# Performance work log

Measured on AMD Instinct MI355X. Metric: run time of the kernel, lower is better.

## Reference

```python
import jax, jax.numpy as jnp
import numpy as np

N_NODES = 100000
N_EDGES = 600000
IN_SIZE = 128
OUT_SIZE = 128
N_GRAPHS = 100
BN_EPS = 1e-5


def setup_inputs() -> dict:
    key = jax.random.key(0)
    ks = jax.random.split(key, 8)
    h = jax.random.normal(ks[0], (N_NODES, IN_SIZE), dtype=jnp.float32)
    norm = jax.random.uniform(ks[1], (N_NODES, 1), dtype=jnp.float32)
    src = jax.random.randint(ks[2], (N_EDGES,), 0, N_NODES, dtype=jnp.int32)
    dst = jax.random.randint(ks[3], (N_EDGES,), 0, N_NODES, dtype=jnp.int32)
    graph_ids = jnp.sort(jax.random.randint(ks[4], (N_NODES,), 0, N_GRAPHS, dtype=jnp.int32))
    # Linear + BatchNorm params
    W = jax.random.normal(ks[5], (IN_SIZE, OUT_SIZE), dtype=jnp.float32) / np.sqrt(IN_SIZE)
    b = jnp.zeros((OUT_SIZE,), dtype=jnp.float32)
    gamma = jnp.ones((OUT_SIZE,), dtype=jnp.float32)
    beta = jnp.zeros((OUT_SIZE,), dtype=jnp.float32)
    return {"h": h, "norm": norm, "W": W, "b": b, "gamma": gamma, "beta": beta,
            "src": src, "dst": dst, "graph_ids": graph_ids}


def reference(h, norm, W, b, gamma, beta, src, dst, graph_ids):
    # pre-normalize, scatter-sum over edges (copy_src + sum), post-normalize
    x = h * norm                                            # [N, in]
    agg = jax.ops.segment_sum(x[src], dst, num_segments=N_NODES)  # SpMM
    x = agg * norm
    # linear + relu
    x = jax.nn.relu(jnp.dot(x, W) + b)                      # [N, out]
    # BatchNorm1d (training-mode: batch mean, biased variance)
    mean = jnp.mean(x, axis=0)
    var = jnp.mean(jnp.square(x - mean), axis=0)
    x = (x - mean) * jax.lax.rsqrt(var + BN_EPS) * gamma + beta
    # sum_nodes pooling per graph
    phis = jax.ops.segment_sum(x, graph_ids, num_segments=N_GRAPHS)  # [G, out]
    return (x, phis)
```

## Files before the change

### kernel.cpp

```cpp
#include <hip/hip_runtime.h>
#include <hip/hip_bf16.h>

#define N_NODES 100000
#define N_PAD 100096
#define N_EDGES 600000
#define CH 128
#define N_GRAPHS 100
#define BN_EPS 1e-5f
#define NBUCKET 64
#define CAP 32
#define OVFCAP 8192
#define FILL_BLOCKS 586
#define PRESCALE_BLOCKS 6250

typedef __bf16 bf16x8 __attribute__((ext_vector_type(8)));
typedef float f32x4 __attribute__((ext_vector_type(4)));

__device__ __forceinline__ ushort f2bf(float f) {
    union { float f; unsigned u; } x; x.f = f;
    unsigned u = x.u;
    unsigned r = (u + 0x7fffu + ((u >> 16) & 1u)) >> 16;
    return (ushort)r;
}
__device__ __forceinline__ float bflo(unsigned p) { return __builtin_bit_cast(float, p << 16); }
__device__ __forceinline__ float bfhi(unsigned p) { return __builtin_bit_cast(float, p & 0xffff0000u); }

__global__ __launch_bounds__(256) void k_front(const int* __restrict__ src,
        const int* __restrict__ dst, const float* __restrict__ h,
        const float* __restrict__ norm, const float* __restrict__ W,
        int* __restrict__ cnt, int* __restrict__ ovfcur, int* __restrict__ ovf,
        int* __restrict__ esrc, ushort* __restrict__ xh, ushort* __restrict__ Wt) {
    unsigned bid = blockIdx.x;
    if (bid < FILL_BLOCKS) {
        int e0 = (bid * 256 + threadIdx.x) * 4;
        if (e0 < N_EDGES) {
            int4 d = *(const int4*)(dst + e0);
            int4 s = *(const int4*)(src + e0);
            int s0 = atomicAdd(&cnt[d.x], 1);
            int s1 = atomicAdd(&cnt[d.y], 1);
            int s2 = atomicAdd(&cnt[d.z], 1);
            int s3 = atomicAdd(&cnt[d.w], 1);
            if (s0 < CAP) esrc[d.x * CAP + s0] = s.x;
            else { int p = atomicAdd(ovfcur, 1); if (p < OVFCAP) { ovf[2*p] = d.x; ovf[2*p+1] = s.x; } }
            if (s1 < CAP) esrc[d.y * CAP + s1] = s.y;
            else { int p = atomicAdd(ovfcur, 1); if (p < OVFCAP) { ovf[2*p] = d.y; ovf[2*p+1] = s.y; } }
            if (s2 < CAP) esrc[d.z * CAP + s2] = s.z;
            else { int p = atomicAdd(ovfcur, 1); if (p < OVFCAP) { ovf[2*p] = d.z; ovf[2*p+1] = s.z; } }
            if (s3 < CAP) esrc[d.w * CAP + s3] = s.w;
            else { int p = atomicAdd(ovfcur, 1); if (p < OVFCAP) { ovf[2*p] = d.w; ovf[2*p+1] = s.w; } }
        }
    } else if (bid < FILL_BLOCKS + PRESCALE_BLOCKS) {
        int t = (bid - FILL_BLOCKS) * 256 + threadIdx.x;
        int n = t >> 4, c = (t & 15) << 3;
        float nm = norm[n];
        float4 a = *(const float4*)(h + (size_t)n * CH + c);
        float4 d = *(const float4*)(h + (size_t)n * CH + c + 4);
        uint4 o;
        o.x = (unsigned)f2bf(a.x * nm) | ((unsigned)f2bf(a.y * nm) << 16);
        o.y = (unsigned)f2bf(a.z * nm) | ((unsigned)f2bf(a.w * nm) << 16);
        o.z = (unsigned)f2bf(d.x * nm) | ((unsigned)f2bf(d.y * nm) << 16);
        o.w = (unsigned)f2bf(d.z * nm) | ((unsigned)f2bf(d.w * nm) << 16);
        *(uint4*)(xh + (size_t)n * CH + c) = o;
    } else {
        int t = (bid - FILL_BLOCKS - PRESCALE_BLOCKS) * 256 + threadIdx.x;
        int k = t >> 7, o = t & 127;
        Wt[o * CH + k] = f2bf(W[t]);
    }
}

__global__ __launch_bounds__(256) void k_gather(const ushort* __restrict__ xh,
        const float* __restrict__ norm, const int* __restrict__ cnt,
        const int* __restrict__ esrc, const int* __restrict__ ovfcur,
        const int* __restrict__ ovf, ushort* __restrict__ x2) {
    int t = blockIdx.x * 256 + threadIdx.x;
    int n = t >> 4;
    int c = (t & 15) << 3;
    if (n >= N_PAD) return;
    int e = 0;
    float nn = 0.f;
    if (n < N_NODES) { e = min(cnt[n], CAP); nn = norm[n]; }
    int base = n * CAP;
    float a0=0.f,a1=0.f,a2=0.f,a3=0.f,a4=0.f,a5=0.f,a6=0.f,a7=0.f;
    int j = 0;
    for (; j + 4 <= e; j += 4) {
        int s0 = esrc[base + j], s1 = esrc[base + j + 1];
        int s2 = esrc[base + j + 2], s3 = esrc[base + j + 3];
        uint4 v0 = *(const uint4*)(xh + (size_t)s0 * CH + c);
        uint4 v1 = *(const uint4*)(xh + (size_t)s1 * CH + c);
        uint4 v2 = *(const uint4*)(xh + (size_t)s2 * CH + c);
        uint4 v3 = *(const uint4*)(xh + (size_t)s3 * CH + c);
        a0 += bflo(v0.x) + bflo(v1.x) + bflo(v2.x) + bflo(v3.x);
        a1 += bfhi(v0.x) + bfhi(v1.x) + bfhi(v2.x) + bfhi(v3.x);
        a2 += bflo(v0.y) + bflo(v1.y) + bflo(v2.y) + bflo(v3.y);
        a3 += bfhi(v0.y) + bfhi(v1.y) + bfhi(v2.y) + bfhi(v3.y);
        a4 += bflo(v0.z) + bflo(v1.z) + bflo(v2.z) + bflo(v3.z);
        a5 += bfhi(v0.z) + bfhi(v1.z) + bfhi(v2.z) + bfhi(v3.z);
        a6 += bflo(v0.w) + bflo(v1.w) + bflo(v2.w) + bflo(v3.w);
        a7 += bfhi(v0.w) + bfhi(v1.w) + bfhi(v2.w) + bfhi(v3.w);
    }
    for (; j < e; j++) {
        int s = esrc[base + j];
        uint4 v = *(const uint4*)(xh + (size_t)s * CH + c);
        a0 += bflo(v.x); a1 += bfhi(v.x);
        a2 += bflo(v.y); a3 += bfhi(v.y);
        a4 += bflo(v.z); a5 += bfhi(v.z);
        a6 += bflo(v.w); a7 += bfhi(v.w);
    }
    if (n < N_NODES) {
        int no = *ovfcur;
        if (no > 0) {
            no = min(no, OVFCAP);
            for (int i = 0; i < no; i++) {
                if (ovf[2*i] == n) {
                    int s = ovf[2*i+1];
                    uint4 v = *(const uint4*)(xh + (size_t)s * CH + c);
                    a0 += bflo(v.x); a1 += bfhi(v.x);
                    a2 += bflo(v.y); a3 += bfhi(v.y);
                    a4 += bflo(v.z); a5 += bfhi(v.z);
                    a6 += bflo(v.w); a7 += bfhi(v.w);
                }
            }
        }
    }
    uint4 o;
    o.x = (unsigned)f2bf(a0 * nn) | ((unsigned)f2bf(a1 * nn) << 16);
    o.y = (unsigned)f2bf(a2 * nn) | ((unsigned)f2bf(a3 * nn) << 16);
    o.z = (unsigned)f2bf(a4 * nn) | ((unsigned)f2bf(a5 * nn) << 16);
    o.w = (unsigned)f2bf(a6 * nn) | ((unsigned)f2bf(a7 * nn) << 16);
    *(uint4*)(x2 + (size_t)n * CH + c) = o;
}

__global__ __launch_bounds__(256) void k_gemm(const ushort* __restrict__ x2,
        const ushort* __restrict__ Wt, const float* __restrict__ bias,
        ushort* __restrict__ y16, float* __restrict__ psum, float* __restrict__ psq) {
    __shared__ ushort ys[128 * CH];

    int tid = threadIdx.x;
    int w = tid >> 6, L = tid & 63;
    int c15 = L & 15, quad = L >> 4;
    size_t nb = (size_t)blockIdx.x * 128 + w * 32;

    const bf16x8* A0 = (const bf16x8*)(x2 + (nb + c15) * CH);
    const bf16x8* A1 = (const bf16x8*)(x2 + (nb + 16 + c15) * CH);

    f32x4 acc0[8] = {}, acc1[8] = {};
    #pragma unroll
    for (int kt = 0; kt < 4; kt++) {
        bf16x8 a0 = A0[kt * 4 + quad];
        bf16x8 a1 = A1[kt * 4 + quad];
        #pragma unroll
        for (int ot = 0; ot < 8; ot++) {
            bf16x8 b = *(const bf16x8*)(Wt + (size_t)(ot * 16 + c15) * CH + kt * 32 + quad * 8);
            acc0[ot] = __builtin_amdgcn_mfma_f32_16x16x32_bf16(a0, b, acc0[ot], 0, 0, 0);
            acc1[ot] = __builtin_amdgcn_mfma_f32_16x16x32_bf16(a1, b, acc1[ot], 0, 0, 0);
        }
    }

    float sA[8], qA[8];
    #pragma unroll
    for (int ot = 0; ot < 8; ot++) {
        int col = ot * 16 + c15;
        float bv = bias[col];
        float s_ = 0.f, q_ = 0.f;
        #pragma unroll
        for (int r = 0; r < 4; r++) {
            size_t n = nb + quad * 4 + r;
            float v = fmaxf(acc0[ot][r] + bv, 0.f);
            ys[(w * 32 + quad * 4 + r) * CH + col] = f2bf(v);
            if (n < N_NODES) { s_ += v; q_ += v * v; }
            size_t n2 = n + 16;
            float v2 = fmaxf(acc1[ot][r] + bv, 0.f);
            ys[(w * 32 + 16 + quad * 4 + r) * CH + col] = f2bf(v2);
            if (n2 < N_NODES) { s_ += v2; q_ += v2 * v2; }
        }
        sA[ot] = s_; qA[ot] = q_;
    }
    __syncthreads();

    {
        const uint4* ysv = (const uint4*)ys;
        uint4* out = (uint4*)(y16 + (size_t)blockIdx.x * 128 * CH);
        #pragma unroll
        for (int i = 0; i < 8; i++) out[tid + i * 256] = ysv[tid + i * 256];
    }
    __syncthreads();

    float* red = (float*)ys;
    #pragma unroll
    for (int ot = 0; ot < 8; ot++) {
        red[ot * 256 + tid] = sA[ot];
        red[2048 + ot * 256 + tid] = qA[ot];
    }
    __syncthreads();

    if (tid < 128) {
        int ot = tid >> 4, cc = tid & 15;
        int col = ot * 16 + cc;
        float S = 0.f, Q = 0.f;
        #pragma unroll
        for (int g = 0; g < 16; g++) {
            int sl = (g >> 2) * 64 + (g & 3) * 16 + cc;
            S += red[ot * 256 + sl];
            Q += red[2048 + ot * 256 + sl];
        }
        int bucket = blockIdx.x & (NBUCKET - 1);
        atomicAdd(&psum[bucket * CH + col], S);
        atomicAdd(&psq[bucket * CH + col], Q);
    }
}

__global__ void k_finalize(const float* __restrict__ psum, const float* __restrict__ psq,
        const float* __restrict__ gamma, const float* __restrict__ beta,
        float* __restrict__ scale, float* __restrict__ shift, float* __restrict__ phis) {
    int t = threadIdx.x;
    float S = 0.f, Q = 0.f;
    for (int g = 0; g < NBUCKET; g++) { S += psum[g * CH + t]; Q += psq[g * CH + t]; }
    const float invN = 1.f / (float)N_NODES;
    float mean = S * invN;
    float var  = Q * invN - mean * mean;
    float sc   = gamma[t] * rsqrtf(var + BN_EPS);
    scale[t] = sc;
    shift[t] = beta[t] - mean * sc;
    for (int i = t; i < N_GRAPHS * CH; i += 128) phis[i] = 0.f;
}

__global__ __launch_bounds__(256) void k_bnpool(const ushort* __restrict__ y16,
        const int* __restrict__ gids, const float* __restrict__ scale,
        const float* __restrict__ shift, float* __restrict__ xout,
        float* __restrict__ phis) {
    __shared__ float smP[16][CH];

    int tid = threadIdx.x;
    int cg = tid & 15, rl = tid >> 4;
    int c = cg * 8;
    int r0 = blockIdx.x * 256;
    int rbase = r0 + rl * 16;

    float4 sc0 = *(const float4*)(scale + c), sc1 = *(const float4*)(scale + c + 4);
    float4 sh0 = *(const float4*)(shift + c), sh1 = *(const float4*)(shift + c + 4);

    bool fast = (r0 + 255 < N_NODES) && (gids[r0] == gids[r0 + 255]);

    if (fast) {
        float4 p0 = make_float4(0.f,0.f,0.f,0.f), p1 = make_float4(0.f,0.f,0.f,0.f);
        for (int j = 0; j < 16; j++) {
            int r = rbase + j;
            uint4 v = *(const uint4*)(y16 + (size_t)r * CH + c);
            float4 f0, f1;
            f0.x = fmaf(bflo(v.x), sc0.x, sh0.x); f0.y = fmaf(bfhi(v.x), sc0.y, sh0.y);
            f0.z = fmaf(bflo(v.y), sc0.z, sh0.z); f0.w = fmaf(bfhi(v.y), sc0.w, sh0.w);
            f1.x = fmaf(bflo(v.z), sc1.x, sh1.x); f1.y = fmaf(bfhi(v.z), sc1.y, sh1.y);
            f1.z = fmaf(bflo(v.w), sc1.z, sh1.z); f1.w = fmaf(bfhi(v.w), sc1.w, sh1.w);
            *(float4*)(xout + (size_t)r * CH + c) = f0;
            *(float4*)(xout + (size_t)r * CH + c + 4) = f1;
            p0.x += f0.x; p0.y += f0.y; p0.z += f0.z; p0.w += f0.w;
            p1.x += f1.x; p1.y += f1.y; p1.z += f1.z; p1.w += f1.w;
        }
        *(float4*)&smP[rl][c] = p0;
        *(float4*)&smP[rl][c + 4] = p1;
        __syncthreads();
        if (tid < 128) {
            int g = gids[r0];
            float S = 0.f;
            #pragma unroll
            for (int k = 0; k < 16; k++) S += smP[k][tid];
            atomicAdd(&phis[(size_t)g * CH + tid], S);
        }
    } else {
        float p[8] = {};
        int gprev = -1;
        for (int j = 0; j < 16; j++) {
            int r = rbase + j;
            if (r >= N_NODES) break;
            int g = gids[r];
            if (g != gprev) {
                if (gprev >= 0) {
                    #pragma unroll
                    for (int k = 0; k < 8; k++) {
                        atomicAdd(&phis[(size_t)gprev * CH + c + k], p[k]);
                        p[k] = 0.f;
                    }
                }
                gprev = g;
            }
            uint4 v = *(const uint4*)(y16 + (size_t)r * CH + c);
            float f[8];
            f[0] = fmaf(bflo(v.x), sc0.x, sh0.x); f[1] = fmaf(bfhi(v.x), sc0.y, sh0.y);
            f[2] = fmaf(bflo(v.y), sc0.z, sh0.z); f[3] = fmaf(bfhi(v.y), sc0.w, sh0.w);
            f[4] = fmaf(bflo(v.z), sc1.x, sh1.x); f[5] = fmaf(bfhi(v.z), sc1.y, sh1.y);
            f[6] = fmaf(bflo(v.w), sc1.z, sh1.z); f[7] = fmaf(bfhi(v.w), sc1.w, sh1.w);
            *(float4*)(xout + (size_t)r * CH + c) = make_float4(f[0], f[1], f[2], f[3]);
            *(float4*)(xout + (size_t)r * CH + c + 4) = make_float4(f[4], f[5], f[6], f[7]);
            #pragma unroll
            for (int k = 0; k < 8; k++) p[k] += f[k];
        }
        if (gprev >= 0) {
            #pragma unroll
            for (int k = 0; k < 8; k++)
                atomicAdd(&phis[(size_t)gprev * CH + c + k], p[k]);
        }
    }
}

extern "C" void kernel_launch(void* const* d_in, const int* in_sizes, int n_in,
                              void* d_out, int out_size, void* d_ws, size_t ws_size,
                              hipStream_t stream)
{
    const float* h     = (const float*)d_in[0];
    const float* norm  = (const float*)d_in[1];
    const float* W     = (const float*)d_in[2];
    const float* b     = (const float*)d_in[3];
    const float* gamma = (const float*)d_in[4];
    const float* beta  = (const float*)d_in[5];
    const int*   src   = (const int*)d_in[6];
    const int*   dst   = (const int*)d_in[7];
    const int*   gids  = (const int*)d_in[8];

    float* x_out = (float*)d_out;
    float* phis  = x_out + (size_t)N_NODES * CH;

    ushort* xh   = (ushort*)d_ws;
    ushort* x2   = xh + (size_t)N_NODES * CH;
    ushort* y16  = x2 + (size_t)N_PAD * CH;
    ushort* Wt   = y16 + (size_t)N_PAD * CH;
    int*   cnt     = (int*)(Wt + CH * CH);
    float* psum    = (float*)(cnt + N_NODES);
    float* psq     = psum + NBUCKET * CH;
    int*   ovfcur  = (int*)(psq + NBUCKET * CH);
    int*   esrc    = ovfcur + 4;
    int*   ovf     = esrc + (size_t)N_NODES * CAP;
    float* scale   = (float*)(ovf + 2 * OVFCAP);
    float* shift   = scale + CH;

    hipMemsetAsync(cnt, 0, (size_t)(N_NODES + 2 * NBUCKET * CH + 4) * sizeof(int), stream);

    k_front<<<FILL_BLOCKS + PRESCALE_BLOCKS + 64, 256, 0, stream>>>(
        src, dst, h, norm, W, cnt, ovfcur, ovf, esrc, xh, Wt);
    k_gather<<<N_PAD / 16, 256, 0, stream>>>(xh, norm, cnt, esrc, ovfcur, ovf, x2);
    k_gemm<<<N_PAD / 128, 256, 0, stream>>>(x2, Wt, b, y16, psum, psq);
    k_finalize<<<1, 128, 0, stream>>>(psum, psq, gamma, beta, scale, shift, phis);
    k_bnpool<<<(N_NODES + 255) / 256, 256, 0, stream>>>(y16, gids, scale, shift, x_out, phis);
}
```

Baseline: 229.2 us.

## Split front kernel, fold memset into prep, shrink CAP, grid-stride gather

Replaces the hipMemsetAsync with zeroing blocks inside a new prep kernel, which also clears phis. The edge fill becomes its own kernel with one edge per thread and nontemporal stores. CAP is halved to 16 so the esrc table and its memory traffic shrink, and overflow scans now run only for nodes above capacity. The gather becomes grid-stride and loads four indices at once, and bnpool processes 64 rows per block for more parallelism. The risks are serial overflow scans in the gather whenever many nodes exceed 16 edges, and more atomics on phis from the smaller pooling blocks.

```diff
diff --git a/kernel.cpp b/kernel.cpp
--- a/kernel.cpp
+++ b/kernel.cpp
@@ -7,10 +7,17 @@
 #define CH 128
 #define N_GRAPHS 100
 #define BN_EPS 1e-5f
-#define NBUCKET 64
-#define CAP 32
+#define NBUCKET 32
+#define CAP 16
 #define OVFCAP 8192
-#define FILL_BLOCKS 586
+#define EDGE_BLOCKS 2344
+#define GEMM_BLOCKS 782
+#define GATHER_BLOCKS 2048
+#define BN_BLOCKS 1563
+#define ZERO_INTS (N_NODES + 2 * NBUCKET * CH + 4)
+#define ZERO_BLOCKS 423
+#define PHIS_BLOCKS 50
+#define WT_BLOCKS 64
 #define PRESCALE_BLOCKS 6250
 
 typedef __bf16 bf16x8 __attribute__((ext_vector_type(8)));
@@ -25,32 +32,24 @@
 __device__ __forceinline__ float bflo(unsigned p) { return __builtin_bit_cast(float, p << 16); }
 __device__ __forceinline__ float bfhi(unsigned p) { return __builtin_bit_cast(float, p & 0xffff0000u); }
 
-__global__ __launch_bounds__(256) void k_front(const int* __restrict__ src,
-        const int* __restrict__ dst, const float* __restrict__ h,
-        const float* __restrict__ norm, const float* __restrict__ W,
-        int* __restrict__ cnt, int* __restrict__ ovfcur, int* __restrict__ ovf,
-        int* __restrict__ esrc, ushort* __restrict__ xh, ushort* __restrict__ Wt) {
+__global__ __launch_bounds__(256) void k_prep(const float* __restrict__ W,
+        const float* __restrict__ h, const float* __restrict__ norm,
+        int* __restrict__ zbase, ushort* __restrict__ Wt,
+        float* __restrict__ phis, ushort* __restrict__ xh) {
     unsigned bid = blockIdx.x;
-    if (bid < FILL_BLOCKS) {
-        int e0 = (bid * 256 + threadIdx.x) * 4;
-        if (e0 < N_EDGES) {
-            int4 d = *(const int4*)(dst + e0);
-            int4 s = *(const int4*)(src + e0);
-            int s0 = atomicAdd(&cnt[d.x], 1);
-            int s1 = atomicAdd(&cnt[d.y], 1);
-            int s2 = atomicAdd(&cnt[d.z], 1);
-            int s3 = atomicAdd(&cnt[d.w], 1);
-            if (s0 < CAP) esrc[d.x * CAP + s0] = s.x;
-            else { int p = atomicAdd(ovfcur, 1); if (p < OVFCAP) { ovf[2*p] = d.x; ovf[2*p+1] = s.x; } }
-            if (s1 < CAP) esrc[d.y * CAP + s1] = s.y;
-            else { int p = atomicAdd(ovfcur, 1); if (p < OVFCAP) { ovf[2*p] = d.y; ovf[2*p+1] = s.y; } }
-            if (s2 < CAP) esrc[d.z * CAP + s2] = s.z;
-            else { int p = atomicAdd(ovfcur, 1); if (p < OVFCAP) { ovf[2*p] = d.z; ovf[2*p+1] = s.z; } }
-            if (s3 < CAP) esrc[d.w * CAP + s3] = s.w;
-            else { int p = atomicAdd(ovfcur, 1); if (p < OVFCAP) { ovf[2*p] = d.w; ovf[2*p+1] = s.w; } }
-        }
-    } else if (bid < FILL_BLOCKS + PRESCALE_BLOCKS) {
-        int t = (bid - FILL_BLOCKS) * 256 + threadIdx.x;
+    int tid = threadIdx.x;
+    if (bid < ZERO_BLOCKS) {
+        int i = bid * 256 + tid;
+        if (i < ZERO_INTS) zbase[i] = 0;
+    } else if (bid < ZERO_BLOCKS + PHIS_BLOCKS) {
+        int i = (bid - ZERO_BLOCKS) * 256 + tid;
+        phis[i] = 0.f;
+    } else if (bid < ZERO_BLOCKS + PHIS_BLOCKS + WT_BLOCKS) {
+        int t = (bid - ZERO_BLOCKS - PHIS_BLOCKS) * 256 + tid;
+        int k = t >> 7, o = t & 127;
+        Wt[o * CH + k] = f2bf(W[t]);
+    } else {
+        int t = (bid - ZERO_BLOCKS - PHIS_BLOCKS - WT_BLOCKS) * 256 + tid;
         int n = t >> 4, c = (t & 15) << 3;
         float nm = norm[n];
         float4 a = *(const float4*)(h + (size_t)n * CH + c);
@@ -61,10 +60,18 @@
         o.z = (unsigned)f2bf(d.x * nm) | ((unsigned)f2bf(d.y * nm) << 16);
         o.w = (unsigned)f2bf(d.z * nm) | ((unsigned)f2bf(d.w * nm) << 16);
         *(uint4*)(xh + (size_t)n * CH + c) = o;
-    } else {
-        int t = (bid - FILL_BLOCKS - PRESCALE_BLOCKS) * 256 + threadIdx.x;
-        int k = t >> 7, o = t & 127;
-        Wt[o * CH + k] = f2bf(W[t]);
+    }
+}
+
+__global__ __launch_bounds__(256) void k_fill(const int* __restrict__ src,
+        const int* __restrict__ dst, int* __restrict__ cnt,
+        int* __restrict__ ovfcur, int* __restrict__ ovf, int* __restrict__ esrc) {
+    int e = blockIdx.x * 256 + threadIdx.x;
+    if (e < N_EDGES) {
+        int d = dst[e], s = src[e];
+        int slot = atomicAdd(&cnt[d], 1);
+        if (slot < CAP) __builtin_nontemporal_store(s, &esrc[d * CAP + slot]);
+        else { int p = atomicAdd(ovfcur, 1); if (p < OVFCAP) { ovf[2*p] = d; ovf[2*p+1] = s; } }
     }
 }
 
@@ -72,44 +79,47 @@
         const float* __restrict__ norm, const int* __restrict__ cnt,
         const int* __restrict__ esrc, const int* __restrict__ ovfcur,
         const int* __restrict__ ovf, ushort* __restrict__ x2) {
-    int t = blockIdx.x * 256 + threadIdx.x;
-    int n = t >> 4;
-    int c = (t & 15) << 3;
-    if (n >= N_PAD) return;
-    int e = 0;
-    float nn = 0.f;
-    if (n < N_NODES) { e = min(cnt[n], CAP); nn = norm[n]; }
-    int base = n * CAP;
-    float a0=0.f,a1=0.f,a2=0.f,a3=0.f,a4=0.f,a5=0.f,a6=0.f,a7=0.f;
-    int j = 0;
-    for (; j + 4 <= e; j += 4) {
-        int s0 = esrc[base + j], s1 = esrc[base + j + 1];
-        int s2 = esrc[base + j + 2], s3 = esrc[base + j + 3];
-        uint4 v0 = *(const uint4*)(xh + (size_t)s0 * CH + c);
-        uint4 v1 = *(const uint4*)(xh + (size_t)s1 * CH + c);
-        uint4 v2 = *(const uint4*)(xh + (size_t)s2 * CH + c);
-        uint4 v3 = *(const uint4*)(xh + (size_t)s3 * CH + c);
-        a0 += bflo(v0.x) + bflo(v1.x) + bflo(v2.x) + bflo(v3.x);
-        a1 += bfhi(v0.x) + bfhi(v1.x) + bfhi(v2.x) + bfhi(v3.x);
-        a2 += bflo(v0.y) + bflo(v1.y) + bflo(v2.y) + bflo(v3.y);
-        a3 += bfhi(v0.y) + bfhi(v1.y) + bfhi(v2.y) + bfhi(v3.y);
-        a4 += bflo(v0.z) + bflo(v1.z) + bflo(v2.z) + bflo(v3.z);
-        a5 += bfhi(v0.z) + bfhi(v1.z) + bfhi(v2.z) + bfhi(v3.z);
-        a6 += bflo(v0.w) + bflo(v1.w) + bflo(v2.w) + bflo(v3.w);
-        a7 += bfhi(v0.w) + bfhi(v1.w) + bfhi(v2.w) + bfhi(v3.w);
-    }
-    for (; j < e; j++) {
-        int s = esrc[base + j];
-        uint4 v = *(const uint4*)(xh + (size_t)s * CH + c);
-        a0 += bflo(v.x); a1 += bfhi(v.x);
-        a2 += bflo(v.y); a3 += bfhi(v.y);
-        a4 += bflo(v.z); a5 += bfhi(v.z);
-        a6 += bflo(v.w); a7 += bfhi(v.w);
-    }
-    if (n < N_NODES) {
-        int no = *ovfcur;
-        if (no > 0) {
-            no = min(no, OVFCAP);
+    int tid = threadIdx.x;
+    int cg = tid & 15, rl = tid >> 4;
+    int c = cg * 8;
+    int no = min(*ovfcur, OVFCAP);
+
+    for (int n = blockIdx.x * 16 + rl; n < N_PAD; n += GATHER_BLOCKS * 16) {
+        if (n >= N_NODES) {
+            uint4 z = {0u, 0u, 0u, 0u};
+            *(uint4*)(x2 + (size_t)n * CH + c) = z;
+            continue;
+        }
+        int craw = cnt[n];
+        int e = min(craw, CAP);
+        float nn = norm[n];
+        int base = n * CAP;
+        float a0=0.f,a1=0.f,a2=0.f,a3=0.f,a4=0.f,a5=0.f,a6=0.f,a7=0.f;
+        int j = 0;
+        for (; j + 4 <= e; j += 4) {
+            int4 s4 = *(const int4*)(esrc + base + j);
+            uint4 v0 = *(const uint4*)(xh + (size_t)s4.x * CH + c);
+            uint4 v1 = *(const uint4*)(xh + (size_t)s4.y * CH + c);
+            uint4 v2 = *(const uint4*)(xh + (size_t)s4.z * CH + c);
+            uint4 v3 = *(const uint4*)(xh + (size_t)s4.w * CH + c);
+            a0 += bflo(v0.x) + bflo(v1.x) + bflo(v2.x) + bflo(v3.x);
+            a1 += bfhi(v0.x) + bfhi(v1.x) + bfhi(v2.x) + bfhi(v3.x);
+            a2 += bflo(v0.y) + bflo(v1.y) + bflo(v2.y) + bflo(v3.y);
+            a3 += bfhi(v0.y) + bfhi(v1.y) + bfhi(v2.y) + bfhi(v3.y);
+            a4 += bflo(v0.z) + bflo(v1.z) + bflo(v2.z) + bflo(v3.z);
+            a5 += bfhi(v0.z) + bfhi(v1.z) + bfhi(v2.z) + bfhi(v3.z);
+            a6 += bflo(v0.w) + bflo(v1.w) + bflo(v2.w) + bflo(v3.w);
+            a7 += bfhi(v0.w) + bfhi(v1.w) + bfhi(v2.w) + bfhi(v3.w);
+        }
+        for (; j < e; j++) {
+            int s = esrc[base + j];
+            uint4 v = *(const uint4*)(xh + (size_t)s * CH + c);
+            a0 += bflo(v.x); a1 += bfhi(v.x);
+            a2 += bflo(v.y); a3 += bfhi(v.y);
+            a4 += bflo(v.z); a5 += bfhi(v.z);
+            a6 += bflo(v.w); a7 += bfhi(v.w);
+        }
+        if (craw > CAP && no > 0) {
             for (int i = 0; i < no; i++) {
                 if (ovf[2*i] == n) {
                     int s = ovf[2*i+1];
@@ -121,13 +131,13 @@
                 }
             }
         }
-    }
-    uint4 o;
-    o.x = (unsigned)f2bf(a0 * nn) | ((unsigned)f2bf(a1 * nn) << 16);
-    o.y = (unsigned)f2bf(a2 * nn) | ((unsigned)f2bf(a3 * nn) << 16);
-    o.z = (unsigned)f2bf(a4 * nn) | ((unsigned)f2bf(a5 * nn) << 16);
-    o.w = (unsigned)f2bf(a6 * nn) | ((unsigned)f2bf(a7 * nn) << 16);
-    *(uint4*)(x2 + (size_t)n * CH + c) = o;
+        uint4 o;
+        o.x = (unsigned)f2bf(a0 * nn) | ((unsigned)f2bf(a1 * nn) << 16);
+        o.y = (unsigned)f2bf(a2 * nn) | ((unsigned)f2bf(a3 * nn) << 16);
+        o.z = (unsigned)f2bf(a4 * nn) | ((unsigned)f2bf(a5 * nn) << 16);
+        o.w = (unsigned)f2bf(a6 * nn) | ((unsigned)f2bf(a7 * nn) << 16);
+        *(uint4*)(x2 + (size_t)n * CH + c) = o;
+    }
 }
 
 __global__ __launch_bounds__(256) void k_gemm(const ushort* __restrict__ x2,
@@ -211,9 +221,10 @@
 
 __global__ void k_finalize(const float* __restrict__ psum, const float* __restrict__ psq,
         const float* __restrict__ gamma, const float* __restrict__ beta,
-        float* __restrict__ scale, float* __restrict__ shift, float* __restrict__ phis) {
+        float* __restrict__ scale, float* __restrict__ shift) {
     int t = threadIdx.x;
     float S = 0.f, Q = 0.f;
+    #pragma unroll
     for (int g = 0; g < NBUCKET; g++) { S += psum[g * CH + t]; Q += psq[g * CH + t]; }
     const float invN = 1.f / (float)N_NODES;
     float mean = S * invN;
@@ -221,7 +232,6 @@
     float sc   = gamma[t] * rsqrtf(var + BN_EPS);
     scale[t] = sc;
     shift[t] = beta[t] - mean * sc;
-    for (int i = t; i < N_GRAPHS * CH; i += 128) phis[i] = 0.f;
 }
 
 __global__ __launch_bounds__(256) void k_bnpool(const ushort* __restrict__ y16,
@@ -233,17 +243,18 @@
     int tid = threadIdx.x;
     int cg = tid & 15, rl = tid >> 4;
     int c = cg * 8;
-    int r0 = blockIdx.x * 256;
-    int rbase = r0 + rl * 16;
+    int r0 = blockIdx.x * 64;
+    int rbase = r0 + rl * 4;
 
     float4 sc0 = *(const float4*)(scale + c), sc1 = *(const float4*)(scale + c + 4);
     float4 sh0 = *(const float4*)(shift + c), sh1 = *(const float4*)(shift + c + 4);
 
-    bool fast = (r0 + 255 < N_NODES) && (gids[r0] == gids[r0 + 255]);
+    bool fast = (r0 + 63 < N_NODES) && (gids[r0] == gids[r0 + 63]);
 
     if (fast) {
         float4 p0 = make_float4(0.f,0.f,0.f,0.f), p1 = make_float4(0.f,0.f,0.f,0.f);
-        for (int j = 0; j < 16; j++) {
+        #pragma unroll
+        for (int j = 0; j < 4; j++) {
             int r = rbase + j;
             uint4 v = *(const uint4*)(y16 + (size_t)r * CH + c);
             float4 f0, f1;
@@ -269,7 +280,8 @@
     } else {
         float p[8] = {};
         int gprev = -1;
-        for (int j = 0; j < 16; j++) {
+        #pragma unroll
+        for (int j = 0; j < 4; j++) {
             int r = rbase + j;
             if (r >= N_NODES) break;
             int g = gids[r];
@@ -332,12 +344,13 @@
     float* scale   = (float*)(ovf + 2 * OVFCAP);
     float* shift   = scale + CH;
 
-    hipMemsetAsync(cnt, 0, (size_t)(N_NODES + 2 * NBUCKET * CH + 4) * sizeof(int), stream);
-
-    k_front<<<FILL_BLOCKS + PRESCALE_BLOCKS + 64, 256, 0, stream>>>(
-        src, dst, h, norm, W, cnt, ovfcur, ovf, esrc, xh, Wt);
-    k_gather<<<N_PAD / 16, 256, 0, stream>>>(xh, norm, cnt, esrc, ovfcur, ovf, x2);
-    k_gemm<<<N_PAD / 128, 256, 0, stream>>>(x2, Wt, b, y16, psum, psq);
-    k_finalize<<<1, 128, 0, stream>>>(psum, psq, gamma, beta, scale, shift, phis);
-    k_bnpool<<<(N_NODES + 255) / 256, 256, 0, stream>>>(y16, gids, scale, shift, x_out, phis);
-}
+    k_prep<<<ZERO_BLOCKS + PHIS_BLOCKS + WT_BLOCKS + PRESCALE_BLOCKS, 256, 0, stream>>>(
+        W, h, norm, cnt, Wt, phis, xh);
+    k_fill<<<EDGE_BLOCKS, 256, 0, stream>>>(src, dst, cnt, ovfcur, ovf, esrc);
+    k_gather<<<GATHER_BLOCKS, 256, 0, stream>>>(
+        xh, norm, cnt, esrc, ovfcur, ovf, x2);
+    k_gemm<<<GEMM_BLOCKS, 256, 0, stream>>>(x2, Wt, b, y16, psum, psq);
+    k_finalize<<<1, 128, 0, stream>>>(psum, psq, gamma, beta, scale, shift);
+    k_bnpool<<<BN_BLOCKS, 256, 0, stream>>>(
+        y16, gids, scale, shift, x_out, phis);
+}
```

Result: no change. 230.6 us (+0.6%).
